# Performance work log

Measured on AMD Instinct MI355X. Metric: run time of the kernel, lower is better.

## Reference

```python
import jax, jax.numpy as jnp
import numpy as np

NEG = -9e15
SLOPE = 0.02

def setup_inputs() -> dict:
    key = jax.random.key(0)
    k1, k2, k3, k4 = jax.random.split(key, 4)
    N, IN, OUT = 16384, 128, 64
    x = jax.random.normal(k1, (N, IN), dtype=jnp.float32)
    adj = jax.random.randint(k2, (N, N), 0, 2, dtype=jnp.int32)
    weight = jax.random.normal(k3, (IN, OUT), dtype=jnp.float32) * (1.0 / np.sqrt(IN))
    att_weight = jax.random.normal(k4, (2 * OUT, 1), dtype=jnp.float32) * (1.0 / np.sqrt(2 * OUT))
    return {"x": x, "adj": adj, "weight": weight, "att_weight": att_weight}

def reference(x, adj, weight, att_weight):
    out_feature = weight.shape[1]
    Wh = x @ weight                                   # [N, out]
    f_i = Wh @ att_weight[:out_feature, :]            # [N, 1] source term
    f_j = Wh @ att_weight[out_feature:, :]            # [N, 1] dest term
    e = f_i + f_j.T                                   # [N, N] additive scores
    e = jax.nn.leaky_relu(e, negative_slope=SLOPE)
    att = jnp.where(adj > 0, e, NEG)
    att = jax.nn.softmax(att, axis=1)                 # masked row softmax
    h_prime = att @ Wh                                # [N, out]
    return jax.nn.elu(h_prime)                        # concat=True -> elu
```

## Files before the change

### kernel.cpp

```cpp
#include <hip/hip_runtime.h>
#include <cstdint>
#include <cstddef>

#define GN   16384
#define GIN  128
#define GOUT 64
#define LOG2E 1.44269504088896340736f

typedef __attribute__((ext_vector_type(8))) short short8;
typedef __attribute__((ext_vector_type(4))) float f32x4;
typedef __attribute__((ext_vector_type(4))) int   int4v;

__device__ __forceinline__ unsigned short f2bf(float f) {
  unsigned u = __float_as_uint(f);
  return (unsigned short)((u + 0x8000u) >> 16);
}

__device__ __forceinline__ unsigned short f2bf_rne(float f) {
  unsigned u = __float_as_uint(f);
  u += 0x7FFFu + ((u >> 16) & 1u);
  return (unsigned short)(u >> 16);
}

__global__ __launch_bounds__(256) void prep_kernel(
    const float* __restrict__ x, const float* __restrict__ w,
    const float* __restrict__ aw, unsigned short* __restrict__ wpk,
    float* __restrict__ fs2, float* __restrict__ fd2)
{
  __shared__ float ws[GIN * GOUT];
  __shared__ float red[2][64][4];

  const int t = threadIdx.x;
  const int rb = blockIdx.x * 64;

  for (int i = t; i < (GIN * GOUT) / 4; i += 256)
    ((float4*)ws)[i] = ((const float4*)w)[i];
  __syncthreads();

  const int r = t & 63, s = t >> 6;
  const int row = rb + r;
  const float* xr = x + (size_t)row * GIN;

  float acc[16];
#pragma unroll
  for (int d = 0; d < 16; ++d) acc[d] = 0.f;

  for (int kk = 0; kk < GIN; kk += 4) {
    float4 xv = *(const float4*)(xr + kk);
    float xa[4] = {xv.x, xv.y, xv.z, xv.w};
#pragma unroll
    for (int u = 0; u < 4; ++u) {
#pragma unroll
      for (int d = 0; d < 16; ++d)
        acc[d] += xa[u] * ws[(kk + u) * GOUT + s * 16 + d];
    }
  }

  const int jc = row >> 5;
  const int qq = (row & 31) >> 3;
  const int tt = row & 7;
  float psrc = 0.f, pdst = 0.f;
#pragma unroll
  for (int d = 0; d < 16; ++d) {
    const int dg = s * 16 + d;
    psrc += acc[d] * aw[dg];
    pdst += acc[d] * aw[GOUT + dg];
    const int f = dg >> 4, n = dg & 15;
    wpk[(size_t)jc * 4096 + f * 1024 + (qq * 16 + n) * 8 + tt] = f2bf_rne(acc[d]);
  }
  red[0][r][s] = psrc;
  red[1][r][s] = pdst;
  __syncthreads();
  if (s == 0) {
    float a_ = red[0][r][0] + red[0][r][1] + red[0][r][2] + red[0][r][3];
    float b_ = red[1][r][0] + red[1][r][1] + red[1][r][2] + red[1][r][3];
    fs2[row] = a_ * LOG2E;
    fd2[row] = b_ * LOG2E;
  }
}

__global__ __launch_bounds__(256) void gat_main(
    const int* __restrict__ adj, const unsigned short* __restrict__ wpk,
    const float* __restrict__ fs2, const float* __restrict__ fd2,
    float* __restrict__ out)
{
  const int wave  = blockIdx.x * 4 + (threadIdx.x >> 6);
  const int lane  = threadIdx.x & 63;
  const int m = lane & 15;
  const int q = lane >> 4;
  const int row = wave * 16 + m;

  const float fs = fs2[row];

  const int4v*  __restrict__ arow = (const int4v*)(adj + (size_t)row * GN);
  const float4* __restrict__ fdv  = (const float4*)fd2;
  const short8* __restrict__ wpk8 = (const short8*)wpk;

  f32x4 acc0 = {0,0,0,0}, acc1 = {0,0,0,0}, acc2 = {0,0,0,0}, acc3 = {0,0,0,0};
  f32x4 accd = {0,0,0,0};

  short8 b_ones;
#pragma unroll
  for (int i = 0; i < 8; ++i) b_ones[i] = (short)0x3F80;

  auto pcalc = [&](int a, float fd) -> unsigned short {
    float sv = fs + fd;
    float lv = fmaxf(sv, 0.02f * sv);
    float pe = __builtin_amdgcn_exp2f(lv);
    pe = (a != 0) ? pe : 0.f;
    return f2bf(pe);
  };

#pragma unroll 2
  for (int j = 0; j < GN; j += 32) {
    const int i4 = (j >> 2) + (q << 1);
    int4v a0 = __builtin_nontemporal_load(arow + i4);
    int4v a1 = __builtin_nontemporal_load(arow + i4 + 1);
    float4 f0 = fdv[i4];
    float4 f1 = fdv[i4 + 1];

    const short8* wb = wpk8 + (size_t)(j >> 5) * 512 + lane;
    short8 b0 = wb[0];
    short8 b1 = wb[128];
    short8 b2 = wb[256];
    short8 b3 = wb[384];

    short8 af;
    af[0] = (short)pcalc(a0.x, f0.x);
    af[1] = (short)pcalc(a0.y, f0.y);
    af[2] = (short)pcalc(a0.z, f0.z);
    af[3] = (short)pcalc(a0.w, f0.w);
    af[4] = (short)pcalc(a1.x, f1.x);
    af[5] = (short)pcalc(a1.y, f1.y);
    af[6] = (short)pcalc(a1.z, f1.z);
    af[7] = (short)pcalc(a1.w, f1.w);

    acc0 = __builtin_amdgcn_mfma_f32_16x16x32_bf16(af, b0, acc0, 0, 0, 0);
    acc1 = __builtin_amdgcn_mfma_f32_16x16x32_bf16(af, b1, acc1, 0, 0, 0);
    acc2 = __builtin_amdgcn_mfma_f32_16x16x32_bf16(af, b2, acc2, 0, 0, 0);
    acc3 = __builtin_amdgcn_mfma_f32_16x16x32_bf16(af, b3, acc3, 0, 0, 0);
    accd = __builtin_amdgcn_mfma_f32_16x16x32_bf16(af, b_ones, accd, 0, 0, 0);
  }

  const int orow0 = wave * 16 + q * 4;
#pragma unroll
  for (int r = 0; r < 4; ++r) {
    const float dv = accd[r];
    float* orow = out + (size_t)(orow0 + r) * GOUT + m;
    float v0 = acc0[r] / dv;
    float v1 = acc1[r] / dv;
    float v2 = acc2[r] / dv;
    float v3 = acc3[r] / dv;
    orow[0]  = (v0 > 0.f) ? v0 : expm1f(v0);
    orow[16] = (v1 > 0.f) ? v1 : expm1f(v1);
    orow[32] = (v2 > 0.f) ? v2 : expm1f(v2);
    orow[48] = (v3 > 0.f) ? v3 : expm1f(v3);
  }
}

extern "C" void kernel_launch(void* const* d_in, const int* in_sizes, int n_in,
                              void* d_out, int out_size, void* d_ws, size_t ws_size,
                              hipStream_t stream) {
  const float* x   = (const float*)d_in[0];
  const int*   adj = (const int*)d_in[1];
  const float* w   = (const float*)d_in[2];
  const float* aw  = (const float*)d_in[3];
  float* out = (float*)d_out;

  float* fs2 = (float*)d_ws;
  float* fd2 = fs2 + GN;
  unsigned short* wpk = (unsigned short*)(fd2 + GN);

  prep_kernel<<<GN / 64, 256, 0, stream>>>(x, w, aw, wpk, fs2, fd2);
  gat_main<<<256, 256, 0, stream>>>(adj, wpk, fs2, fd2, out);
}
```

Measured before the change: 1.553 ms.

## Split GAT columns into two chunks with LDS double-buffered adjacency staging

The main kernel now splits the neighbour dimension into two halves across 1024 blocks of two waves each. It writes partial numerators and denominators to workspace, and a new finalize kernel combines them and applies ELU. Adjacency tiles are loaded as coalesced row segments into a double-buffered LDS tile, so global loads run ahead of the exp/MFMA work. The aim is more waves in flight and better latency hiding on the 1 GiB adjacency stream. The cost is extra workspace traffic, a third kernel launch, and LDS staging overhead.

```diff
diff --git a/kernel.cpp b/kernel.cpp
--- a/kernel.cpp
+++ b/kernel.cpp
@@ -5,11 +5,16 @@
 #define GN   16384
 #define GIN  128
 #define GOUT 64
+#define NCH  2
+#define CT   128
+#define LROW 128
+#define TILES ((GN / NCH) / CT)
 #define LOG2E 1.44269504088896340736f
 
 typedef __attribute__((ext_vector_type(8))) short short8;
 typedef __attribute__((ext_vector_type(4))) float f32x4;
 typedef __attribute__((ext_vector_type(4))) int   int4v;
+typedef __attribute__((ext_vector_type(2))) int   int2v;
 
 __device__ __forceinline__ unsigned short f2bf(float f) {
   unsigned u = __float_as_uint(f);
@@ -79,22 +84,26 @@
   }
 }
 
-__global__ __launch_bounds__(256) void gat_main(
+__global__ __launch_bounds__(128) void gat_main(
     const int* __restrict__ adj, const unsigned short* __restrict__ wpk,
     const float* __restrict__ fs2, const float* __restrict__ fd2,
-    float* __restrict__ out)
+    float* __restrict__ nump, float* __restrict__ denp)
 {
-  const int wave  = blockIdx.x * 4 + (threadIdx.x >> 6);
-  const int lane  = threadIdx.x & 63;
+  __shared__ int lbuf[2 * 2 * 16 * LROW];
+
+  const int widx = threadIdx.x >> 6;
+  const int lane = threadIdx.x & 63;
+  const int chunk = blockIdx.x >> 9;
+  const int strip = (blockIdx.x & 511) * 2 + widx;
   const int m = lane & 15;
   const int q = lane >> 4;
-  const int row = wave * 16 + m;
-
-  const float fs = fs2[row];
-
-  const int4v*  __restrict__ arow = (const int4v*)(adj + (size_t)row * GN);
-  const float4* __restrict__ fdv  = (const float4*)fd2;
-  const short8* __restrict__ wpk8 = (const short8*)wpk;
+  const int j0 = chunk * (GN / NCH);
+
+  const float fs = fs2[strip * 16 + m];
+  const int*    __restrict__ abase = adj + (size_t)(strip * 16) * GN + lane * 2;
+  const float4* __restrict__ fdv   = (const float4*)fd2;
+  const short8* __restrict__ wpk8  = (const short8*)wpk;
+  int* lw = lbuf + widx * (2 * 16 * LROW);
 
   f32x4 acc0 = {0,0,0,0}, acc1 = {0,0,0,0}, acc2 = {0,0,0,0}, acc3 = {0,0,0,0};
   f32x4 accd = {0,0,0,0};
@@ -111,51 +120,93 @@
     return f2bf(pe);
   };
 
-#pragma unroll 2
-  for (int j = 0; j < GN; j += 32) {
-    const int i4 = (j >> 2) + (q << 1);
-    int4v a0 = __builtin_nontemporal_load(arow + i4);
-    int4v a1 = __builtin_nontemporal_load(arow + i4 + 1);
-    float4 f0 = fdv[i4];
-    float4 f1 = fdv[i4 + 1];
-
-    const short8* wb = wpk8 + (size_t)(j >> 5) * 512 + lane;
-    short8 b0 = wb[0];
-    short8 b1 = wb[128];
-    short8 b2 = wb[256];
-    short8 b3 = wb[384];
-
-    short8 af;
-    af[0] = (short)pcalc(a0.x, f0.x);
-    af[1] = (short)pcalc(a0.y, f0.y);
-    af[2] = (short)pcalc(a0.z, f0.z);
-    af[3] = (short)pcalc(a0.w, f0.w);
-    af[4] = (short)pcalc(a1.x, f1.x);
-    af[5] = (short)pcalc(a1.y, f1.y);
-    af[6] = (short)pcalc(a1.z, f1.z);
-    af[7] = (short)pcalc(a1.w, f1.w);
-
-    acc0 = __builtin_amdgcn_mfma_f32_16x16x32_bf16(af, b0, acc0, 0, 0, 0);
-    acc1 = __builtin_amdgcn_mfma_f32_16x16x32_bf16(af, b1, acc1, 0, 0, 0);
-    acc2 = __builtin_amdgcn_mfma_f32_16x16x32_bf16(af, b2, acc2, 0, 0, 0);
-    acc3 = __builtin_amdgcn_mfma_f32_16x16x32_bf16(af, b3, acc3, 0, 0, 0);
-    accd = __builtin_amdgcn_mfma_f32_16x16x32_bf16(af, b_ones, accd, 0, 0, 0);
-  }
-
-  const int orow0 = wave * 16 + q * 4;
+  int2v stage[16];
+  auto load_tile = [&](int jt) {
+#pragma unroll
+    for (int r = 0; r < 16; ++r)
+      stage[r] = __builtin_nontemporal_load((const int2v*)(abase + (size_t)r * GN + jt));
+  };
+  auto write_tile = [&](int b) {
+    int* ld = lw + b * (16 * LROW) + lane * 2;
+#pragma unroll
+    for (int r = 0; r < 16; ++r)
+      *(int2v*)(ld + r * LROW) = stage[r];
+  };
+
+  load_tile(j0);
+  write_tile(0);
+
+  for (int t = 0; t < TILES; ++t) {
+    const int jt = j0 + t * CT;
+    const int buf = t & 1;
+
+    short8 bw[4][4];
+    float4 ff[4][2];
+#pragma unroll
+    for (int jj = 0; jj < 4; ++jj) {
+      const int j = jt + jj * 32;
+      const short8* wb = wpk8 + (size_t)(j >> 5) * 512 + lane;
+      bw[jj][0] = wb[0];
+      bw[jj][1] = wb[128];
+      bw[jj][2] = wb[256];
+      bw[jj][3] = wb[384];
+      const int i4 = (j >> 2) + (q << 1);
+      ff[jj][0] = fdv[i4];
+      ff[jj][1] = fdv[i4 + 1];
+    }
+
+    if (t + 1 < TILES) load_tile(jt + CT);
+
+    const int* lsrc = lw + buf * (16 * LROW) + m * LROW + q * 8;
+#pragma unroll
+    for (int jj = 0; jj < 4; ++jj) {
+      int4v a0 = *(const int4v*)(lsrc + jj * 32);
+      int4v a1 = *(const int4v*)(lsrc + jj * 32 + 4);
+      float4 f0 = ff[jj][0], f1 = ff[jj][1];
+      short8 af;
+      af[0] = (short)pcalc(a0.x, f0.x);
+      af[1] = (short)pcalc(a0.y, f0.y);
+      af[2] = (short)pcalc(a0.z, f0.z);
+      af[3] = (short)pcalc(a0.w, f0.w);
+      af[4] = (short)pcalc(a1.x, f1.x);
+      af[5] = (short)pcalc(a1.y, f1.y);
+      af[6] = (short)pcalc(a1.z, f1.z);
+      af[7] = (short)pcalc(a1.w, f1.w);
+      acc0 = __builtin_amdgcn_mfma_f32_16x16x32_bf16(af, bw[jj][0], acc0, 0, 0, 0);
+      acc1 = __builtin_amdgcn_mfma_f32_16x16x32_bf16(af, bw[jj][1], acc1, 0, 0, 0);
+      acc2 = __builtin_amdgcn_mfma_f32_16x16x32_bf16(af, bw[jj][2], acc2, 0, 0, 0);
+      acc3 = __builtin_amdgcn_mfma_f32_16x16x32_bf16(af, bw[jj][3], acc3, 0, 0, 0);
+      accd = __builtin_amdgcn_mfma_f32_16x16x32_bf16(af, b_ones, accd, 0, 0, 0);
+    }
+
+    if (t + 1 < TILES) write_tile(buf ^ 1);
+  }
+
+  float* np = nump + (size_t)chunk * GN * GOUT;
+  float* dp = denp + (size_t)chunk * GN;
+  const int orow0 = strip * 16 + q * 4;
 #pragma unroll
   for (int r = 0; r < 4; ++r) {
-    const float dv = accd[r];
-    float* orow = out + (size_t)(orow0 + r) * GOUT + m;
-    float v0 = acc0[r] / dv;
-    float v1 = acc1[r] / dv;
-    float v2 = acc2[r] / dv;
-    float v3 = acc3[r] / dv;
-    orow[0]  = (v0 > 0.f) ? v0 : expm1f(v0);
-    orow[16] = (v1 > 0.f) ? v1 : expm1f(v1);
-    orow[32] = (v2 > 0.f) ? v2 : expm1f(v2);
-    orow[48] = (v3 > 0.f) ? v3 : expm1f(v3);
-  }
+    float* nr = np + (size_t)(orow0 + r) * GOUT + m;
+    __builtin_nontemporal_store(acc0[r], nr + 0);
+    __builtin_nontemporal_store(acc1[r], nr + 16);
+    __builtin_nontemporal_store(acc2[r], nr + 32);
+    __builtin_nontemporal_store(acc3[r], nr + 48);
+    if (m == 0) dp[orow0 + r] = accd[r];
+  }
+}
+
+__global__ __launch_bounds__(256) void fin_kernel(
+    const float* __restrict__ nump, const float* __restrict__ denp,
+    float* __restrict__ out)
+{
+  const int g = blockIdx.x * 256 + threadIdx.x;
+  if (g >= GN * GOUT) return;
+  const int row = g >> 6;
+  float s = nump[g] + nump[(size_t)GN * GOUT + g];
+  float d = denp[row] + denp[GN + row];
+  float v = s / d;
+  out[g] = (v > 0.f) ? v : expm1f(v);
 }
 
 extern "C" void kernel_launch(void* const* d_in, const int* in_sizes, int n_in,
@@ -167,10 +218,13 @@
   const float* aw  = (const float*)d_in[3];
   float* out = (float*)d_out;
 
-  float* fs2 = (float*)d_ws;
-  float* fd2 = fs2 + GN;
+  float* nump = (float*)d_ws;
+  float* denp = nump + (size_t)NCH * GN * GOUT;
+  float* fs2  = denp + (size_t)NCH * GN;
+  float* fd2  = fs2 + GN;
   unsigned short* wpk = (unsigned short*)(fd2 + GN);
 
   prep_kernel<<<GN / 64, 256, 0, stream>>>(x, w, aw, wpk, fs2, fd2);
-  gat_main<<<256, 256, 0, stream>>>(adj, wpk, fs2, fd2, out);
-}
+  gat_main<<<1024, 128, 0, stream>>>(adj, wpk, fs2, fd2, nump, denp);
+  fin_kernel<<<(GN * GOUT) / 256, 256, 0, stream>>>(nump, denp, out);
+}
```

New measurement: 1.391 ms. 1.12x faster.
